# Kernel tuning notes

Measured on AMD Instinct MI355X. Metric: run time of the kernel, lower is better.

Reference implementation:

```python
import jax, jax.numpy as jnp
import numpy as np

EPS = 1e-5


def setup_inputs() -> dict:
    key = jax.random.key(0)
    S, B, I, H, D = 256, 512, 64, 128, 32
    ks = jax.random.split(key, 12)

    def w(k, shape, fan):
        return jax.random.normal(k, shape, jnp.float32) * (fan ** -0.5)

    lengths = jax.random.randint(ks[0], (B,), 1, S + 1)
    lengths = lengths.at[0].set(S)  # ensure max length == S
    return {
        'x': jax.random.normal(ks[1], (S, B, I), jnp.float32),
        'x_d': jax.random.normal(ks[2], (S, B, D), jnp.float32),
        'lengths': lengths,
        'bn_g': jnp.ones((I,), jnp.float32), 'bn_b': jnp.zeros((I,), jnp.float32),
        'bnd_g': jnp.ones((D,), jnp.float32), 'bnd_b': jnp.zeros((D,), jnp.float32),
        'Wih': w(ks[3], (3 * H, I), I), 'Whh': w(ks[4], (3 * H, H), H),
        'bih': jnp.zeros((3 * H,), jnp.float32), 'bhh': jnp.zeros((3 * H,), jnp.float32),
        'attn_W': w(ks[5], (H, H), H), 'attn_b': jnp.zeros((H,), jnp.float32),
        'W1': w(ks[6], (H, H + D), H + D), 'b1': jnp.zeros((H,), jnp.float32),
        'W2': w(ks[7], (H, H), H), 'b2': jnp.zeros((H,), jnp.float32),
        'W3': w(ks[8], (H, H), H), 'b3': jnp.zeros((H,), jnp.float32),
    }


def reference(x, x_d, lengths, bn_g, bn_b, bnd_g, bnd_b, Wih, Whh, bih, bhh,
              attn_W, attn_b, W1, b1, W2, b2, W3, b3):
    S, B, I = x.shape
    H = Whh.shape[1]
    mask = jnp.arange(S)[:, None] < lengths[None, :]          # [S,B] valid-token mask
    mf = mask[..., None].astype(x.dtype)                       # [S,B,1]
    cnt = mf.sum()

    def bn(v, g, b):  # training-mode BatchNorm1d over the packed (valid) tokens
        mu = (v * mf).sum((0, 1)) / cnt
        var = (((v - mu) * mf) ** 2).sum((0, 1)) / cnt
        return (v - mu) * jax.lax.rsqrt(var + EPS) * g + b

    xn = bn(x, bn_g, bn_b)
    xdn = bn(x_d, bnd_g, bnd_b)

    # --- GRU (PyTorch gate order r,z,n) over padded sequence with mask ---
    h0 = jnp.zeros((B, H), x.dtype)

    def step(h, inp):
        xt, mt = inp                                           # xt [B,I], mt [B,1]
        gi = xt @ Wih.T + bih
        gh = h @ Whh.T + bhh
        ir, iz, inn = jnp.split(gi, 3, axis=-1)
        hr, hz, hn = jnp.split(gh, 3, axis=-1)
        r = jax.nn.sigmoid(ir + hr)
        z = jax.nn.sigmoid(iz + hz)
        n = jnp.tanh(inn + r * hn)
        hnew = (1 - z) * n + z * h
        hnext = jnp.where(mt, hnew, h)                         # carry last valid state
        return hnext, jnp.where(mt, hnew, 0.0)                 # padded outputs are 0

    h_last, ys = jax.lax.scan(step, h0, (xn, mf))              # ys [S,B,H]

    # --- Dynamic_Attention: per step i only position j=i survives the causal
    # mask in column k=i, so the dim-0 softmax is over one element -> weight 1.
    # Keep fc in the graph (zero grad, same as torch) via a size-1 softmax. ---
    s = (ys @ attn_W.T + attn_b).sum(-1)                       # [S,B]
    attn = jax.nn.softmax(s[..., None, None], axis=-2)[..., 0, :]  # ones [S,B,1]
    y = attn * ys

    # --- per-token MLP (dropout = identity at eval), vectorized over all tokens ---
    z0 = jnp.concatenate([y, xdn], axis=-1)                    # [S,B,H+D]
    d = jax.nn.relu(z0 @ W1.T + b1)
    d = jax.nn.relu(d @ W2.T + b2)
    d = jax.nn.relu(d @ W3.T + b3)
    out = d * mf                                               # zero padded positions
    return out, h_last[None]                                   # hidden: [1,B,H]
```

## Files before the change

kernel.cpp:

```cpp
#include <hip/hip_runtime.h>
#include <hip/hip_bf16.h>

#define SS 256
#define BB 512
#define II 64
#define HH 128
#define DD 32

typedef __attribute__((ext_vector_type(8))) short short8;
typedef __attribute__((ext_vector_type(4))) float f32x4;

__device__ __forceinline__ short f2bf(float f) {
    unsigned u = __builtin_bit_cast(unsigned, f);
    u += 0x7FFFu + ((u >> 16) & 1u);
    return (short)(u >> 16);
}
__device__ __forceinline__ int pack2bf(float a, float b) {
    return (int)((((unsigned)(unsigned short)f2bf(b)) << 16) |
                  ((unsigned)(unsigned short)f2bf(a)));
}
__device__ __forceinline__ short8 load8bf(const float* p) {
    short8 r;
#pragma unroll
    for (int j = 0; j < 8; ++j) r[j] = f2bf(p[j]);
    return r;
}

__device__ __forceinline__ void sync_lds() {
    __builtin_amdgcn_s_waitcnt(0xc07f);
    __builtin_amdgcn_s_barrier();
}

__global__ __launch_bounds__(256) void stats_kernel(
    const float* __restrict__ x, const float* __restrict__ xd,
    const int* __restrict__ lengths, double* __restrict__ acc,
    unsigned* __restrict__ counter,
    const float* __restrict__ bn_g, const float* __restrict__ bn_b,
    const float* __restrict__ bnd_g, const float* __restrict__ bnd_b,
    float* __restrict__ der)
{
    __shared__ int s_len[BB];
    __shared__ f32x4 red_s[256];
    __shared__ f32x4 red_q[256];
    __shared__ unsigned s_last;

    const int tid = threadIdx.x;
    const int blk = blockIdx.x;
    for (int i = tid; i < BB; i += 256) s_len[i] = lengths[i];
    __syncthreads();

    f32x4 s = {0.f, 0.f, 0.f, 0.f};
    f32x4 q = {0.f, 0.f, 0.f, 0.f};

    if (blk < 256) {
        const int c4   = tid & 15;
        const int rowg = tid >> 4;
        const float* base = x + (size_t)blk * BB * II + c4 * 4;
#pragma unroll 8
        for (int it = 0; it < 32; ++it) {
            const int b = it * 16 + rowg;
            const f32x4 xv = *(const f32x4*)&base[(size_t)b * II];
            const f32x4 xm = (blk < s_len[b]) ? xv : (f32x4){0.f, 0.f, 0.f, 0.f};
            s += xm;
            q += xm * xm;
        }
        red_s[tid] = s; red_q[tid] = q;
        __syncthreads();
#pragma unroll
        for (int g = 8; g >= 1; g >>= 1) {
            if (rowg < g) {
                red_s[tid] += red_s[tid + 16 * g];
                red_q[tid] += red_q[tid + 16 * g];
            }
            __syncthreads();
        }
        if (rowg == 0) {
            const f32x4 fs = red_s[tid], fq = red_q[tid];
#pragma unroll
            for (int j = 0; j < 4; ++j) {
                atomicAdd(&acc[c4 * 4 + j],      (double)fs[j]);
                atomicAdd(&acc[64 + c4 * 4 + j], (double)fq[j]);
            }
        }
    } else {
        const int bx   = blk - 256;
        const int c4   = tid & 7;
        const int rowg = tid >> 3;
        const int r0   = bx * 1024;
        const float* base = xd + (size_t)r0 * DD + c4 * 4;
#pragma unroll 8
        for (int it = 0; it < 32; ++it) {
            const int rr  = it * 32 + rowg;
            const int row = r0 + rr;
            const int b   = row & (BB - 1);
            const int si  = row >> 9;
            const f32x4 xv = *(const f32x4*)&base[(size_t)rr * DD];
            const f32x4 xm = (si < s_len[b]) ? xv : (f32x4){0.f, 0.f, 0.f, 0.f};
            s += xm;
            q += xm * xm;
        }
        red_s[tid] = s; red_q[tid] = q;
        __syncthreads();
#pragma unroll
        for (int g = 16; g >= 1; g >>= 1) {
            if (rowg < g) {
                red_s[tid] += red_s[tid + 8 * g];
                red_q[tid] += red_q[tid + 8 * g];
            }
            __syncthreads();
        }
        if (rowg == 0) {
            const f32x4 fs = red_s[tid], fq = red_q[tid];
#pragma unroll
            for (int j = 0; j < 4; ++j) {
                atomicAdd(&acc[128 + c4 * 4 + j], (double)fs[j]);
                atomicAdd(&acc[160 + c4 * 4 + j], (double)fq[j]);
            }
        }
    }

    __threadfence();
    __syncthreads();
    if (tid == 0) {
        unsigned old = atomicAdd(counter, 1u);
        s_last = (old == 383u) ? 1u : 0u;
    }
    __syncthreads();
    if (!s_last) return;

    __shared__ int redc[256];
    int cs = 0;
    for (int i = tid; i < BB; i += 256) cs += s_len[i];
    redc[tid] = cs;
    __syncthreads();
    for (int off = 128; off; off >>= 1) {
        if (tid < off) redc[tid] += redc[tid + off];
        __syncthreads();
    }
    const double inv = 1.0 / (double)redc[0];
    if (tid < 64) {
        const double su = __hip_atomic_load(&acc[tid],      __ATOMIC_RELAXED, __HIP_MEMORY_SCOPE_AGENT);
        const double sq = __hip_atomic_load(&acc[64 + tid], __ATOMIC_RELAXED, __HIP_MEMORY_SCOPE_AGENT);
        const double mu  = su * inv;
        const double var = sq * inv - mu * mu;
        const float  rs  = rsqrtf((float)(var + 1e-5));
        const float  a   = rs * bn_g[tid];
        der[tid]      = a;
        der[64 + tid] = bn_b[tid] - (float)mu * a;
    } else if (tid < 96) {
        const int i = tid - 64;
        const double su = __hip_atomic_load(&acc[128 + i], __ATOMIC_RELAXED, __HIP_MEMORY_SCOPE_AGENT);
        const double sq = __hip_atomic_load(&acc[160 + i], __ATOMIC_RELAXED, __HIP_MEMORY_SCOPE_AGENT);
        const double mu  = su * inv;
        const double var = sq * inv - mu * mu;
        const float  rs  = rsqrtf((float)(var + 1e-5));
        const float  a   = rs * bnd_g[i];
        der[128 + i] = a;
        der[160 + i] = bnd_b[i] - (float)mu * a;
    }
}

__global__ __launch_bounds__(512, 2) void gru_kernel(
    const float* __restrict__ x, const int* __restrict__ lengths,
    const float* __restrict__ Wih, const float* __restrict__ Whh,
    const float* __restrict__ bih, const float* __restrict__ bhh,
    const float* __restrict__ der,
    float* __restrict__ ys, float* __restrict__ hlast)
{
    __shared__ __align__(16) short hbf[2][16 * 136];
    __shared__ __align__(16) short xbf[2][16 * 72];

    const int tid  = threadIdx.x;
    const int w    = tid >> 6;
    const int l    = tid & 63;
    const int col  = l & 15;
    const int quad = l >> 4;
    const int b0   = blockIdx.x * 16;
    const int ur   = 16 * w + col;
    const int g0   = 16 * w + quad * 4;

    short8 WR[6], WZ[6], WNh[4], WNx[2];
#pragma unroll
    for (int ks = 0; ks < 4; ++ks) {
        const int ko = ks * 32 + quad * 8;
        WR[ks]  = load8bf(&Whh[(size_t)ur * HH + ko]);
        WZ[ks]  = load8bf(&Whh[(size_t)(HH + ur) * HH + ko]);
        WNh[ks] = load8bf(&Whh[(size_t)(2 * HH + ur) * HH + ko]);
    }
#pragma unroll
    for (int ks = 0; ks < 2; ++ks) {
        const int ko = ks * 32 + quad * 8;
        WR[4 + ks] = load8bf(&Wih[(size_t)ur * II + ko]);
        WZ[4 + ks] = load8bf(&Wih[(size_t)(HH + ur) * II + ko]);
        WNx[ks]    = load8bf(&Wih[(size_t)(2 * HH + ur) * II + ko]);
    }
    float br_[4], bz_[4], bnh_[4], bnx_[4];
#pragma unroll
    for (int r = 0; r < 4; ++r) {
        const int g = g0 + r;
        br_[r]  = bih[g] + bhh[g];
        bz_[r]  = bih[HH + g] + bhh[HH + g];
        bnh_[r] = bhh[2 * HH + g];
        bnx_[r] = bih[2 * HH + g];
    }
    const int len = lengths[b0 + col];

    const int srow = tid >> 5, scol = (tid & 31) * 2;
    const float ax0 = der[scol],      ax1 = der[scol + 1];
    const float cx0 = der[64 + scol], cx1 = der[64 + scol + 1];

    for (int i = tid; i < 16 * 136 / 2; i += 512) ((int*)hbf[0])[i] = 0;
    float hreg[4] = {0.f, 0.f, 0.f, 0.f};
    {
        const float2 xv = *(const float2*)&x[(size_t)(b0 + srow) * II + scol];
        *(int*)&xbf[0][srow * 72 + scol] =
            pack2bf(fmaf(xv.x, ax0, cx0), fmaf(xv.y, ax1, cx1));
    }
    sync_lds();

    int p = 0;
    for (int t = 0; t < SS; ++t) {
        float2 xv;
        if (t + 1 < SS)
            xv = *(const float2*)&x[(size_t)((t + 1) * BB + b0 + srow) * II + scol];

        short8 Hf[4];
#pragma unroll
        for (int ks = 0; ks < 4; ++ks)
            Hf[ks] = *(const short8*)&hbf[p][col * 136 + ks * 32 + quad * 8];
        const short8 XN0 = *(const short8*)&xbf[p][col * 72 + quad * 8];
        const short8 XN1 = *(const short8*)&xbf[p][col * 72 + 32 + quad * 8];

        f32x4 ar  = {br_[0],  br_[1],  br_[2],  br_[3]};
        f32x4 az  = {bz_[0],  bz_[1],  bz_[2],  bz_[3]};
        f32x4 anh = {bnh_[0], bnh_[1], bnh_[2], bnh_[3]};
        f32x4 anx = {bnx_[0], bnx_[1], bnx_[2], bnx_[3]};
#pragma unroll
        for (int ks = 0; ks < 4; ++ks) {
            ar  = __builtin_amdgcn_mfma_f32_16x16x32_bf16(WR[ks],  Hf[ks], ar,  0, 0, 0);
            az  = __builtin_amdgcn_mfma_f32_16x16x32_bf16(WZ[ks],  Hf[ks], az,  0, 0, 0);
            anh = __builtin_amdgcn_mfma_f32_16x16x32_bf16(WNh[ks], Hf[ks], anh, 0, 0, 0);
        }
        ar  = __builtin_amdgcn_mfma_f32_16x16x32_bf16(WR[4],  XN0, ar,  0, 0, 0);
        ar  = __builtin_amdgcn_mfma_f32_16x16x32_bf16(WR[5],  XN1, ar,  0, 0, 0);
        az  = __builtin_amdgcn_mfma_f32_16x16x32_bf16(WZ[4],  XN0, az,  0, 0, 0);
        az  = __builtin_amdgcn_mfma_f32_16x16x32_bf16(WZ[5],  XN1, az,  0, 0, 0);
        anx = __builtin_amdgcn_mfma_f32_16x16x32_bf16(WNx[0], XN0, anx, 0, 0, 0);
        anx = __builtin_amdgcn_mfma_f32_16x16x32_bf16(WNx[1], XN1, anx, 0, 0, 0);

        const bool valid = (t < len);
#pragma unroll
        for (int r = 0; r < 4; ++r) {
            const float rg = __builtin_amdgcn_rcpf(1.f + __expf(-ar[r]));
            const float zg = __builtin_amdgcn_rcpf(1.f + __expf(-az[r]));
            const float nv = anx[r] + rg * anh[r];
            const float ng = 1.f - 2.f * __builtin_amdgcn_rcpf(1.f + __expf(2.f * nv));
            const float hnew = (1.f - zg) * ng + zg * hreg[r];
            hreg[r] = valid ? hnew : hreg[r];
        }
        {
            float4 o;
            o.x = hreg[0]; o.y = hreg[1]; o.z = hreg[2]; o.w = hreg[3];
            *(float4*)&ys[((size_t)t * BB + b0 + col) * HH + g0] = o;
            int2 pk;
            pk.x = pack2bf(hreg[0], hreg[1]);
            pk.y = pack2bf(hreg[2], hreg[3]);
            *(int2*)&hbf[p ^ 1][col * 136 + g0] = pk;
        }
        if (t + 1 < SS)
            *(int*)&xbf[p ^ 1][srow * 72 + scol] =
                pack2bf(fmaf(xv.x, ax0, cx0), fmaf(xv.y, ax1, cx1));

        sync_lds();
        p ^= 1;
    }

    {
        float4 hl;
        hl.x = hreg[0]; hl.y = hreg[1]; hl.z = hreg[2]; hl.w = hreg[3];
        *(float4*)&hlast[(size_t)(b0 + col) * HH + g0] = hl;
    }
}

__global__ __launch_bounds__(512, 2) void mlp_kernel(
    const float* __restrict__ xd, const int* __restrict__ lengths,
    const float* __restrict__ W1, const float* __restrict__ b1v,
    const float* __restrict__ W2, const float* __restrict__ b2v,
    const float* __restrict__ W3, const float* __restrict__ b3v,
    const float* __restrict__ der, float* io)
{
    __shared__ __align__(16) short z0[2][16 * 168];
    __shared__ __align__(16) short d1b[2][16 * 136];
    __shared__ __align__(16) short d2b[2][16 * 136];

    const int tid  = threadIdx.x;
    const int w    = tid >> 6;
    const int l    = tid & 63;
    const int col  = l & 15;
    const int quad = l >> 4;
    const int ur   = 16 * w + col;
    const int g0   = 16 * w + quad * 4;

    short8 F1[5], F2[4], F3[4];
#pragma unroll
    for (int ks = 0; ks < 5; ++ks)
        F1[ks] = load8bf(&W1[(size_t)ur * 160 + ks * 32 + quad * 8]);
#pragma unroll
    for (int ks = 0; ks < 4; ++ks) {
        const int ko = ks * 32 + quad * 8;
        F2[ks] = load8bf(&W2[(size_t)ur * HH + ko]);
        F3[ks] = load8bf(&W3[(size_t)ur * HH + ko]);
    }
    float bb1_[4], bb2_[4], bb3_[4];
#pragma unroll
    for (int r = 0; r < 4; ++r) {
        bb1_[r] = b1v[g0 + r]; bb2_[r] = b2v[g0 + r]; bb3_[r] = b3v[g0 + r];
    }

    const int yrow = tid >> 5, yc = (tid & 31) * 4;
    const int drow = tid >> 4, dcol = (tid & 15) * 2;
    float ad0 = 0.f, ad1 = 0.f, cd0 = 0.f, cd1 = 0.f;
    if (tid < 256) {
        ad0 = der[128 + dcol]; ad1 = der[128 + dcol + 1];
        cd0 = der[160 + dcol]; cd1 = der[160 + dcol + 1];
    }

    const int tile0 = blockIdx.x * 16;

    {
        const size_t tok0 = (size_t)tile0 * 16;
        const float4 yv = *(const float4*)&io[(tok0 + yrow) * HH + yc];
        int2 pk;
        pk.x = pack2bf(yv.x, yv.y);
        pk.y = pack2bf(yv.z, yv.w);
        *(int2*)&z0[0][yrow * 168 + yc] = pk;
        if (tid < 256) {
            const float2 dv = *(const float2*)&xd[(tok0 + drow) * DD + dcol];
            *(int*)&z0[0][drow * 168 + HH + dcol] =
                pack2bf(fmaf(dv.x, ad0, cd0), fmaf(dv.y, ad1, cd1));
        }
    }
    sync_lds();

    int p = 0;
    for (int it = 0; it <= 17; ++it) {
        float4 yv; float2 dv;
        const int nt = it + 1;
        if (nt <= 15) {
            const size_t tok0n = (size_t)(tile0 + nt) * 16;
            yv = *(const float4*)&io[(tok0n + yrow) * HH + yc];
            if (tid < 256) dv = *(const float2*)&xd[(tok0n + drow) * DD + dcol];
        }

        f32x4 a1 = {bb1_[0], bb1_[1], bb1_[2], bb1_[3]};
#pragma unroll
        for (int ks = 0; ks < 5; ++ks)
            a1 = __builtin_amdgcn_mfma_f32_16x16x32_bf16(
                F1[ks], *(const short8*)&z0[p][col * 168 + ks * 32 + quad * 8], a1, 0, 0, 0);
        {
            int2 pk;
            pk.x = pack2bf(fmaxf(a1[0], 0.f), fmaxf(a1[1], 0.f));
            pk.y = pack2bf(fmaxf(a1[2], 0.f), fmaxf(a1[3], 0.f));
            *(int2*)&d1b[p ^ 1][col * 136 + g0] = pk;
        }

        f32x4 a2 = {bb2_[0], bb2_[1], bb2_[2], bb2_[3]};
#pragma unroll
        for (int ks = 0; ks < 4; ++ks)
            a2 = __builtin_amdgcn_mfma_f32_16x16x32_bf16(
                F2[ks], *(const short8*)&d1b[p][col * 136 + ks * 32 + quad * 8], a2, 0, 0, 0);
        {
            int2 pk;
            pk.x = pack2bf(fmaxf(a2[0], 0.f), fmaxf(a2[1], 0.f));
            pk.y = pack2bf(fmaxf(a2[2], 0.f), fmaxf(a2[3], 0.f));
            *(int2*)&d2b[p ^ 1][col * 136 + g0] = pk;
        }

        f32x4 a3 = {bb3_[0], bb3_[1], bb3_[2], bb3_[3]};
#pragma unroll
        for (int ks = 0; ks < 4; ++ks)
            a3 = __builtin_amdgcn_mfma_f32_16x16x32_bf16(
                F3[ks], *(const short8*)&d2b[p][col * 136 + ks * 32 + quad * 8], a3, 0, 0, 0);
        if (it >= 2) {
            const int tok0 = (tile0 + it - 2) * 16;
            const int tI = tok0 >> 9;
            const int bI = tok0 & (BB - 1);
            const bool v = tI < lengths[bI + col];
            float4 o;
            o.x = v ? fmaxf(a3[0], 0.f) : 0.f;
            o.y = v ? fmaxf(a3[1], 0.f) : 0.f;
            o.z = v ? fmaxf(a3[2], 0.f) : 0.f;
            o.w = v ? fmaxf(a3[3], 0.f) : 0.f;
            *(float4*)&io[((size_t)tok0 + col) * HH + g0] = o;
        }

        if (nt <= 15) {
            int2 pk;
            pk.x = pack2bf(yv.x, yv.y);
            pk.y = pack2bf(yv.z, yv.w);
            *(int2*)&z0[p ^ 1][yrow * 168 + yc] = pk;
            if (tid < 256)
                *(int*)&z0[p ^ 1][drow * 168 + HH + dcol] =
                    pack2bf(fmaf(dv.x, ad0, cd0), fmaf(dv.y, ad1, cd1));
        }
        sync_lds();
        p ^= 1;
    }
}

extern "C" void kernel_launch(void* const* d_in, const int* in_sizes, int n_in,
                              void* d_out, int out_size, void* d_ws, size_t ws_size,
                              hipStream_t stream)
{
    (void)in_sizes; (void)n_in; (void)out_size; (void)ws_size;
    const float* x     = (const float*)d_in[0];
    const float* xd    = (const float*)d_in[1];
    const int*   lens  = (const int*)d_in[2];
    const float* bn_g  = (const float*)d_in[3];
    const float* bn_b  = (const float*)d_in[4];
    const float* bnd_g = (const float*)d_in[5];
    const float* bnd_b = (const float*)d_in[6];
    const float* Wih   = (const float*)d_in[7];
    const float* Whh   = (const float*)d_in[8];
    const float* bih   = (const float*)d_in[9];
    const float* bhh   = (const float*)d_in[10];
    const float* W1    = (const float*)d_in[13];
    const float* b1    = (const float*)d_in[14];
    const float* W2    = (const float*)d_in[15];
    const float* b2    = (const float*)d_in[16];
    const float* W3    = (const float*)d_in[17];
    const float* b3    = (const float*)d_in[18];

    float* out   = (float*)d_out;
    float* hlast = out + (size_t)SS * BB * HH;

    double*   acc     = (double*)d_ws;
    unsigned* counter = (unsigned*)((char*)d_ws + 1536);
    float*    der     = (float*)((char*)d_ws + 2048);

    (void)hipMemsetAsync(d_ws, 0, 2048, stream);

    stats_kernel<<<384, 256, 0, stream>>>(x, xd, lens, acc, counter,
                                          bn_g, bn_b, bnd_g, bnd_b, der);

    gru_kernel<<<BB / 16, 512, 0, stream>>>(x, lens, Wih, Whh, bih, bhh, der,
                                            out, hlast);

    mlp_kernel<<<512, 512, 0, stream>>>(xd, lens, W1, b1, W2, b2, W3, b3,
                                        der, out);
}
```

Before: 428.8 us.

## Fuse GRU and MLP into one persistent kernel with progress-flag overlap

Merges the GRU and MLP kernels into a single launch. 32 blocks run the recurrence and publish per-block progress counters every 16 timesteps. The remaining 448 blocks spin on those counters and run the MLP on finished time tiles while the recurrence continues, so most of the MLP overlaps the serial GRU. The stats kernel also replaces double atomics with per-block partial sums that the last block reduces. The overlap relies on every GRU block being co-resident with the MLP blocks and uses spin-waits, which risks deadlock or contention with the GRU blocks.

```diff
diff --git a/kernel.cpp b/kernel.cpp
--- a/kernel.cpp
+++ b/kernel.cpp
@@ -33,7 +33,8 @@
 
 __global__ __launch_bounds__(256) void stats_kernel(
     const float* __restrict__ x, const float* __restrict__ xd,
-    const int* __restrict__ lengths, double* __restrict__ acc,
+    const int* __restrict__ lengths,
+    float* __restrict__ px, float* __restrict__ pd,
     unsigned* __restrict__ counter,
     const float* __restrict__ bn_g, const float* __restrict__ bn_b,
     const float* __restrict__ bnd_g, const float* __restrict__ bnd_b,
@@ -76,10 +77,11 @@
         }
         if (rowg == 0) {
             const f32x4 fs = red_s[tid], fq = red_q[tid];
+            float* row = px + (size_t)blk * 128;
 #pragma unroll
             for (int j = 0; j < 4; ++j) {
-                atomicAdd(&acc[c4 * 4 + j],      (double)fs[j]);
-                atomicAdd(&acc[64 + c4 * 4 + j], (double)fq[j]);
+                __hip_atomic_store(&row[c4 * 4 + j],      fs[j], __ATOMIC_RELAXED, __HIP_MEMORY_SCOPE_AGENT);
+                __hip_atomic_store(&row[64 + c4 * 4 + j], fq[j], __ATOMIC_RELAXED, __HIP_MEMORY_SCOPE_AGENT);
             }
         }
     } else {
@@ -111,10 +113,11 @@
         }
         if (rowg == 0) {
             const f32x4 fs = red_s[tid], fq = red_q[tid];
+            float* row = pd + (size_t)bx * 64;
 #pragma unroll
             for (int j = 0; j < 4; ++j) {
-                atomicAdd(&acc[128 + c4 * 4 + j], (double)fs[j]);
-                atomicAdd(&acc[160 + c4 * 4 + j], (double)fq[j]);
+                __hip_atomic_store(&row[c4 * 4 + j],      fs[j], __ATOMIC_RELAXED, __HIP_MEMORY_SCOPE_AGENT);
+                __hip_atomic_store(&row[32 + c4 * 4 + j], fq[j], __ATOMIC_RELAXED, __HIP_MEMORY_SCOPE_AGENT);
             }
         }
     }
@@ -127,7 +130,24 @@
     }
     __syncthreads();
     if (!s_last) return;
-
+    __threadfence();
+
+    __shared__ double s_sum[192];
+    if (tid < 128) {
+        const float* col = px + tid;
+        double a = 0.0;
+#pragma unroll 8
+        for (int r = 0; r < 256; ++r)
+            a += (double)__hip_atomic_load(&col[(size_t)r * 128], __ATOMIC_RELAXED, __HIP_MEMORY_SCOPE_AGENT);
+        s_sum[tid] = a;
+    } else if (tid < 192) {
+        const float* col = pd + (tid - 128);
+        double a = 0.0;
+#pragma unroll 8
+        for (int r = 0; r < 128; ++r)
+            a += (double)__hip_atomic_load(&col[(size_t)r * 64], __ATOMIC_RELAXED, __HIP_MEMORY_SCOPE_AGENT);
+        s_sum[tid] = a;
+    }
     __shared__ int redc[256];
     int cs = 0;
     for (int i = tid; i < BB; i += 256) cs += s_len[i];
@@ -139,20 +159,16 @@
     }
     const double inv = 1.0 / (double)redc[0];
     if (tid < 64) {
-        const double su = __hip_atomic_load(&acc[tid],      __ATOMIC_RELAXED, __HIP_MEMORY_SCOPE_AGENT);
-        const double sq = __hip_atomic_load(&acc[64 + tid], __ATOMIC_RELAXED, __HIP_MEMORY_SCOPE_AGENT);
-        const double mu  = su * inv;
-        const double var = sq * inv - mu * mu;
+        const double mu  = s_sum[tid] * inv;
+        const double var = s_sum[64 + tid] * inv - mu * mu;
         const float  rs  = rsqrtf((float)(var + 1e-5));
         const float  a   = rs * bn_g[tid];
         der[tid]      = a;
         der[64 + tid] = bn_b[tid] - (float)mu * a;
     } else if (tid < 96) {
         const int i = tid - 64;
-        const double su = __hip_atomic_load(&acc[128 + i], __ATOMIC_RELAXED, __HIP_MEMORY_SCOPE_AGENT);
-        const double sq = __hip_atomic_load(&acc[160 + i], __ATOMIC_RELAXED, __HIP_MEMORY_SCOPE_AGENT);
-        const double mu  = su * inv;
-        const double var = sq * inv - mu * mu;
+        const double mu  = s_sum[128 + i] * inv;
+        const double var = s_sum[160 + i] * inv - mu * mu;
         const float  rs  = rsqrtf((float)(var + 1e-5));
         const float  a   = rs * bnd_g[i];
         der[128 + i] = a;
@@ -160,139 +176,19 @@
     }
 }
 
-__global__ __launch_bounds__(512, 2) void gru_kernel(
-    const float* __restrict__ x, const int* __restrict__ lengths,
+__global__ __launch_bounds__(512, 4) void fused_kernel(
+    const float* __restrict__ x, const float* __restrict__ xd,
+    const int* __restrict__ lengths,
     const float* __restrict__ Wih, const float* __restrict__ Whh,
     const float* __restrict__ bih, const float* __restrict__ bhh,
-    const float* __restrict__ der,
-    float* __restrict__ ys, float* __restrict__ hlast)
-{
-    __shared__ __align__(16) short hbf[2][16 * 136];
-    __shared__ __align__(16) short xbf[2][16 * 72];
-
-    const int tid  = threadIdx.x;
-    const int w    = tid >> 6;
-    const int l    = tid & 63;
-    const int col  = l & 15;
-    const int quad = l >> 4;
-    const int b0   = blockIdx.x * 16;
-    const int ur   = 16 * w + col;
-    const int g0   = 16 * w + quad * 4;
-
-    short8 WR[6], WZ[6], WNh[4], WNx[2];
-#pragma unroll
-    for (int ks = 0; ks < 4; ++ks) {
-        const int ko = ks * 32 + quad * 8;
-        WR[ks]  = load8bf(&Whh[(size_t)ur * HH + ko]);
-        WZ[ks]  = load8bf(&Whh[(size_t)(HH + ur) * HH + ko]);
-        WNh[ks] = load8bf(&Whh[(size_t)(2 * HH + ur) * HH + ko]);
-    }
-#pragma unroll
-    for (int ks = 0; ks < 2; ++ks) {
-        const int ko = ks * 32 + quad * 8;
-        WR[4 + ks] = load8bf(&Wih[(size_t)ur * II + ko]);
-        WZ[4 + ks] = load8bf(&Wih[(size_t)(HH + ur) * II + ko]);
-        WNx[ks]    = load8bf(&Wih[(size_t)(2 * HH + ur) * II + ko]);
-    }
-    float br_[4], bz_[4], bnh_[4], bnx_[4];
-#pragma unroll
-    for (int r = 0; r < 4; ++r) {
-        const int g = g0 + r;
-        br_[r]  = bih[g] + bhh[g];
-        bz_[r]  = bih[HH + g] + bhh[HH + g];
-        bnh_[r] = bhh[2 * HH + g];
-        bnx_[r] = bih[2 * HH + g];
-    }
-    const int len = lengths[b0 + col];
-
-    const int srow = tid >> 5, scol = (tid & 31) * 2;
-    const float ax0 = der[scol],      ax1 = der[scol + 1];
-    const float cx0 = der[64 + scol], cx1 = der[64 + scol + 1];
-
-    for (int i = tid; i < 16 * 136 / 2; i += 512) ((int*)hbf[0])[i] = 0;
-    float hreg[4] = {0.f, 0.f, 0.f, 0.f};
-    {
-        const float2 xv = *(const float2*)&x[(size_t)(b0 + srow) * II + scol];
-        *(int*)&xbf[0][srow * 72 + scol] =
-            pack2bf(fmaf(xv.x, ax0, cx0), fmaf(xv.y, ax1, cx1));
-    }
-    sync_lds();
-
-    int p = 0;
-    for (int t = 0; t < SS; ++t) {
-        float2 xv;
-        if (t + 1 < SS)
-            xv = *(const float2*)&x[(size_t)((t + 1) * BB + b0 + srow) * II + scol];
-
-        short8 Hf[4];
-#pragma unroll
-        for (int ks = 0; ks < 4; ++ks)
-            Hf[ks] = *(const short8*)&hbf[p][col * 136 + ks * 32 + quad * 8];
-        const short8 XN0 = *(const short8*)&xbf[p][col * 72 + quad * 8];
-        const short8 XN1 = *(const short8*)&xbf[p][col * 72 + 32 + quad * 8];
-
-        f32x4 ar  = {br_[0],  br_[1],  br_[2],  br_[3]};
-        f32x4 az  = {bz_[0],  bz_[1],  bz_[2],  bz_[3]};
-        f32x4 anh = {bnh_[0], bnh_[1], bnh_[2], bnh_[3]};
-        f32x4 anx = {bnx_[0], bnx_[1], bnx_[2], bnx_[3]};
-#pragma unroll
-        for (int ks = 0; ks < 4; ++ks) {
-            ar  = __builtin_amdgcn_mfma_f32_16x16x32_bf16(WR[ks],  Hf[ks], ar,  0, 0, 0);
-            az  = __builtin_amdgcn_mfma_f32_16x16x32_bf16(WZ[ks],  Hf[ks], az,  0, 0, 0);
-            anh = __builtin_amdgcn_mfma_f32_16x16x32_bf16(WNh[ks], Hf[ks], anh, 0, 0, 0);
-        }
-        ar  = __builtin_amdgcn_mfma_f32_16x16x32_bf16(WR[4],  XN0, ar,  0, 0, 0);
-        ar  = __builtin_amdgcn_mfma_f32_16x16x32_bf16(WR[5],  XN1, ar,  0, 0, 0);
-        az  = __builtin_amdgcn_mfma_f32_16x16x32_bf16(WZ[4],  XN0, az,  0, 0, 0);
-        az  = __builtin_amdgcn_mfma_f32_16x16x32_bf16(WZ[5],  XN1, az,  0, 0, 0);
-        anx = __builtin_amdgcn_mfma_f32_16x16x32_bf16(WNx[0], XN0, anx, 0, 0, 0);
-        anx = __builtin_amdgcn_mfma_f32_16x16x32_bf16(WNx[1], XN1, anx, 0, 0, 0);
-
-        const bool valid = (t < len);
-#pragma unroll
-        for (int r = 0; r < 4; ++r) {
-            const float rg = __builtin_amdgcn_rcpf(1.f + __expf(-ar[r]));
-            const float zg = __builtin_amdgcn_rcpf(1.f + __expf(-az[r]));
-            const float nv = anx[r] + rg * anh[r];
-            const float ng = 1.f - 2.f * __builtin_amdgcn_rcpf(1.f + __expf(2.f * nv));
-            const float hnew = (1.f - zg) * ng + zg * hreg[r];
-            hreg[r] = valid ? hnew : hreg[r];
-        }
-        {
-            float4 o;
-            o.x = hreg[0]; o.y = hreg[1]; o.z = hreg[2]; o.w = hreg[3];
-            *(float4*)&ys[((size_t)t * BB + b0 + col) * HH + g0] = o;
-            int2 pk;
-            pk.x = pack2bf(hreg[0], hreg[1]);
-            pk.y = pack2bf(hreg[2], hreg[3]);
-            *(int2*)&hbf[p ^ 1][col * 136 + g0] = pk;
-        }
-        if (t + 1 < SS)
-            *(int*)&xbf[p ^ 1][srow * 72 + scol] =
-                pack2bf(fmaf(xv.x, ax0, cx0), fmaf(xv.y, ax1, cx1));
-
-        sync_lds();
-        p ^= 1;
-    }
-
-    {
-        float4 hl;
-        hl.x = hreg[0]; hl.y = hreg[1]; hl.z = hreg[2]; hl.w = hreg[3];
-        *(float4*)&hlast[(size_t)(b0 + col) * HH + g0] = hl;
-    }
-}
-
-__global__ __launch_bounds__(512, 2) void mlp_kernel(
-    const float* __restrict__ xd, const int* __restrict__ lengths,
     const float* __restrict__ W1, const float* __restrict__ b1v,
     const float* __restrict__ W2, const float* __restrict__ b2v,
     const float* __restrict__ W3, const float* __restrict__ b3v,
-    const float* __restrict__ der, float* io)
+    const float* __restrict__ der,
+    float* __restrict__ out, float* __restrict__ hlast,
+    int* __restrict__ prog)
 {
-    __shared__ __align__(16) short z0[2][16 * 168];
-    __shared__ __align__(16) short d1b[2][16 * 136];
-    __shared__ __align__(16) short d2b[2][16 * 136];
-
+    __shared__ __align__(16) char smem[28160];
     const int tid  = threadIdx.x;
     const int w    = tid >> 6;
     const int l    = tid & 63;
@@ -301,110 +197,248 @@
     const int ur   = 16 * w + col;
     const int g0   = 16 * w + quad * 4;
 
-    short8 F1[5], F2[4], F3[4];
-#pragma unroll
-    for (int ks = 0; ks < 5; ++ks)
-        F1[ks] = load8bf(&W1[(size_t)ur * 160 + ks * 32 + quad * 8]);
-#pragma unroll
-    for (int ks = 0; ks < 4; ++ks) {
-        const int ko = ks * 32 + quad * 8;
-        F2[ks] = load8bf(&W2[(size_t)ur * HH + ko]);
-        F3[ks] = load8bf(&W3[(size_t)ur * HH + ko]);
-    }
-    float bb1_[4], bb2_[4], bb3_[4];
-#pragma unroll
-    for (int r = 0; r < 4; ++r) {
-        bb1_[r] = b1v[g0 + r]; bb2_[r] = b2v[g0 + r]; bb3_[r] = b3v[g0 + r];
-    }
-
-    const int yrow = tid >> 5, yc = (tid & 31) * 4;
-    const int drow = tid >> 4, dcol = (tid & 15) * 2;
-    float ad0 = 0.f, ad1 = 0.f, cd0 = 0.f, cd1 = 0.f;
-    if (tid < 256) {
-        ad0 = der[128 + dcol]; ad1 = der[128 + dcol + 1];
-        cd0 = der[160 + dcol]; cd1 = der[160 + dcol + 1];
-    }
-
-    const int tile0 = blockIdx.x * 16;
-
-    {
-        const size_t tok0 = (size_t)tile0 * 16;
-        const float4 yv = *(const float4*)&io[(tok0 + yrow) * HH + yc];
-        int2 pk;
-        pk.x = pack2bf(yv.x, yv.y);
-        pk.y = pack2bf(yv.z, yv.w);
-        *(int2*)&z0[0][yrow * 168 + yc] = pk;
+    if (blockIdx.x < 32) {
+        __builtin_amdgcn_s_setprio(2);
+        short (*hbf)[16 * 136] = reinterpret_cast<short (*)[16 * 136]>(smem);
+        short (*xbf)[16 * 72]  = reinterpret_cast<short (*)[16 * 72]>(smem + 8704);
+
+        const int bid = blockIdx.x;
+        const int b0  = bid * 16;
+
+        short8 WR[6], WZ[6], WNh[4], WNx[2];
+#pragma unroll
+        for (int ks = 0; ks < 4; ++ks) {
+            const int ko = ks * 32 + quad * 8;
+            WR[ks]  = load8bf(&Whh[(size_t)ur * HH + ko]);
+            WZ[ks]  = load8bf(&Whh[(size_t)(HH + ur) * HH + ko]);
+            WNh[ks] = load8bf(&Whh[(size_t)(2 * HH + ur) * HH + ko]);
+        }
+#pragma unroll
+        for (int ks = 0; ks < 2; ++ks) {
+            const int ko = ks * 32 + quad * 8;
+            WR[4 + ks] = load8bf(&Wih[(size_t)ur * II + ko]);
+            WZ[4 + ks] = load8bf(&Wih[(size_t)(HH + ur) * II + ko]);
+            WNx[ks]    = load8bf(&Wih[(size_t)(2 * HH + ur) * II + ko]);
+        }
+        float br_[4], bz_[4], bnh_[4], bnx_[4];
+#pragma unroll
+        for (int r = 0; r < 4; ++r) {
+            const int g = g0 + r;
+            br_[r]  = bih[g] + bhh[g];
+            bz_[r]  = bih[HH + g] + bhh[HH + g];
+            bnh_[r] = bhh[2 * HH + g];
+            bnx_[r] = bih[2 * HH + g];
+        }
+        const int len = lengths[b0 + col];
+
+        const int srow = tid >> 5, scol = (tid & 31) * 2;
+        const float ax0 = der[scol],      ax1 = der[scol + 1];
+        const float cx0 = der[64 + scol], cx1 = der[64 + scol + 1];
+
+        for (int i = tid; i < 16 * 136 / 2; i += 512) ((int*)hbf[0])[i] = 0;
+        float hreg[4] = {0.f, 0.f, 0.f, 0.f};
+        {
+            const float2 xv = *(const float2*)&x[(size_t)(b0 + srow) * II + scol];
+            *(int*)&xbf[0][srow * 72 + scol] =
+                pack2bf(fmaf(xv.x, ax0, cx0), fmaf(xv.y, ax1, cx1));
+        }
+        sync_lds();
+
+        int p = 0;
+        for (int t = 0; t < SS; ++t) {
+            float2 xv;
+            if (t + 1 < SS)
+                xv = *(const float2*)&x[(size_t)((t + 1) * BB + b0 + srow) * II + scol];
+
+            short8 Hf[4];
+#pragma unroll
+            for (int ks = 0; ks < 4; ++ks)
+                Hf[ks] = *(const short8*)&hbf[p][col * 136 + ks * 32 + quad * 8];
+            const short8 XN0 = *(const short8*)&xbf[p][col * 72 + quad * 8];
+            const short8 XN1 = *(const short8*)&xbf[p][col * 72 + 32 + quad * 8];
+
+            f32x4 ar  = {br_[0],  br_[1],  br_[2],  br_[3]};
+            f32x4 az  = {bz_[0],  bz_[1],  bz_[2],  bz_[3]};
+            f32x4 anh = {bnh_[0], bnh_[1], bnh_[2], bnh_[3]};
+            f32x4 anx = {bnx_[0], bnx_[1], bnx_[2], bnx_[3]};
+#pragma unroll
+            for (int ks = 0; ks < 4; ++ks) {
+                ar  = __builtin_amdgcn_mfma_f32_16x16x32_bf16(WR[ks],  Hf[ks], ar,  0, 0, 0);
+                az  = __builtin_amdgcn_mfma_f32_16x16x32_bf16(WZ[ks],  Hf[ks], az,  0, 0, 0);
+                anh = __builtin_amdgcn_mfma_f32_16x16x32_bf16(WNh[ks], Hf[ks], anh, 0, 0, 0);
+            }
+            ar  = __builtin_amdgcn_mfma_f32_16x16x32_bf16(WR[4],  XN0, ar,  0, 0, 0);
+            ar  = __builtin_amdgcn_mfma_f32_16x16x32_bf16(WR[5],  XN1, ar,  0, 0, 0);
+            az  = __builtin_amdgcn_mfma_f32_16x16x32_bf16(WZ[4],  XN0, az,  0, 0, 0);
+            az  = __builtin_amdgcn_mfma_f32_16x16x32_bf16(WZ[5],  XN1, az,  0, 0, 0);
+            anx = __builtin_amdgcn_mfma_f32_16x16x32_bf16(WNx[0], XN0, anx, 0, 0, 0);
+            anx = __builtin_amdgcn_mfma_f32_16x16x32_bf16(WNx[1], XN1, anx, 0, 0, 0);
+
+            const bool valid = (t < len);
+#pragma unroll
+            for (int r = 0; r < 4; ++r) {
+                const float rg = __builtin_amdgcn_rcpf(1.f + __expf(-ar[r]));
+                const float zg = __builtin_amdgcn_rcpf(1.f + __expf(-az[r]));
+                const float nv = anx[r] + rg * anh[r];
+                const float ng = 1.f - 2.f * __builtin_amdgcn_rcpf(1.f + __expf(2.f * nv));
+                const float hnew = (1.f - zg) * ng + zg * hreg[r];
+                hreg[r] = valid ? hnew : hreg[r];
+            }
+            {
+                float4 o;
+                o.x = hreg[0]; o.y = hreg[1]; o.z = hreg[2]; o.w = hreg[3];
+                *(float4*)&out[((size_t)t * BB + b0 + col) * HH + g0] = o;
+                int2 pk;
+                pk.x = pack2bf(hreg[0], hreg[1]);
+                pk.y = pack2bf(hreg[2], hreg[3]);
+                *(int2*)&hbf[p ^ 1][col * 136 + g0] = pk;
+            }
+            if (t + 1 < SS)
+                *(int*)&xbf[p ^ 1][srow * 72 + scol] =
+                    pack2bf(fmaf(xv.x, ax0, cx0), fmaf(xv.y, ax1, cx1));
+
+            if ((t & 15) == 15) {
+                asm volatile("s_waitcnt vmcnt(0)" ::: "memory");
+                sync_lds();
+                if (tid == 0) {
+                    __threadfence();
+                    __hip_atomic_store(&prog[bid], t + 1,
+                                       __ATOMIC_RELEASE, __HIP_MEMORY_SCOPE_AGENT);
+                }
+            } else {
+                sync_lds();
+            }
+            p ^= 1;
+        }
+
+        {
+            float4 hl;
+            hl.x = hreg[0]; hl.y = hreg[1]; hl.z = hreg[2]; hl.w = hreg[3];
+            *(float4*)&hlast[(size_t)(b0 + col) * HH + g0] = hl;
+        }
+    } else {
+        short (*z0)[16 * 168]  = reinterpret_cast<short (*)[16 * 168]>(smem);
+        short (*d1b)[16 * 136] = reinterpret_cast<short (*)[16 * 136]>(smem + 10752);
+        short (*d2b)[16 * 136] = reinterpret_cast<short (*)[16 * 136]>(smem + 19456);
+
+        const int j = blockIdx.x - 32;
+
+        short8 F1[5], F2[4], F3[4];
+#pragma unroll
+        for (int ks = 0; ks < 5; ++ks)
+            F1[ks] = load8bf(&W1[(size_t)ur * 160 + ks * 32 + quad * 8]);
+#pragma unroll
+        for (int ks = 0; ks < 4; ++ks) {
+            const int ko = ks * 32 + quad * 8;
+            F2[ks] = load8bf(&W2[(size_t)ur * HH + ko]);
+            F3[ks] = load8bf(&W3[(size_t)ur * HH + ko]);
+        }
+        float bb1_[4], bb2_[4], bb3_[4];
+#pragma unroll
+        for (int r = 0; r < 4; ++r) {
+            bb1_[r] = b1v[g0 + r]; bb2_[r] = b2v[g0 + r]; bb3_[r] = b3v[g0 + r];
+        }
+        const int yrow = tid >> 5, yc = (tid & 31) * 4;
+        const int drow = tid >> 4, dcol = (tid & 15) * 2;
+        float ad0 = 0.f, ad1 = 0.f, cd0 = 0.f, cd1 = 0.f;
         if (tid < 256) {
-            const float2 dv = *(const float2*)&xd[(tok0 + drow) * DD + dcol];
-            *(int*)&z0[0][drow * 168 + HH + dcol] =
-                pack2bf(fmaf(dv.x, ad0, cd0), fmaf(dv.y, ad1, cd1));
-        }
-    }
-    sync_lds();
-
-    int p = 0;
-    for (int it = 0; it <= 17; ++it) {
-        float4 yv; float2 dv;
-        const int nt = it + 1;
-        if (nt <= 15) {
-            const size_t tok0n = (size_t)(tile0 + nt) * 16;
-            yv = *(const float4*)&io[(tok0n + yrow) * HH + yc];
-            if (tid < 256) dv = *(const float2*)&xd[(tok0n + drow) * DD + dcol];
-        }
-
-        f32x4 a1 = {bb1_[0], bb1_[1], bb1_[2], bb1_[3]};
-#pragma unroll
-        for (int ks = 0; ks < 5; ++ks)
-            a1 = __builtin_amdgcn_mfma_f32_16x16x32_bf16(
-                F1[ks], *(const short8*)&z0[p][col * 168 + ks * 32 + quad * 8], a1, 0, 0, 0);
-        {
-            int2 pk;
-            pk.x = pack2bf(fmaxf(a1[0], 0.f), fmaxf(a1[1], 0.f));
-            pk.y = pack2bf(fmaxf(a1[2], 0.f), fmaxf(a1[3], 0.f));
-            *(int2*)&d1b[p ^ 1][col * 136 + g0] = pk;
-        }
-
-        f32x4 a2 = {bb2_[0], bb2_[1], bb2_[2], bb2_[3]};
-#pragma unroll
-        for (int ks = 0; ks < 4; ++ks)
-            a2 = __builtin_amdgcn_mfma_f32_16x16x32_bf16(
-                F2[ks], *(const short8*)&d1b[p][col * 136 + ks * 32 + quad * 8], a2, 0, 0, 0);
-        {
-            int2 pk;
-            pk.x = pack2bf(fmaxf(a2[0], 0.f), fmaxf(a2[1], 0.f));
-            pk.y = pack2bf(fmaxf(a2[2], 0.f), fmaxf(a2[3], 0.f));
-            *(int2*)&d2b[p ^ 1][col * 136 + g0] = pk;
-        }
-
-        f32x4 a3 = {bb3_[0], bb3_[1], bb3_[2], bb3_[3]};
-#pragma unroll
-        for (int ks = 0; ks < 4; ++ks)
-            a3 = __builtin_amdgcn_mfma_f32_16x16x32_bf16(
-                F3[ks], *(const short8*)&d2b[p][col * 136 + ks * 32 + quad * 8], a3, 0, 0, 0);
-        if (it >= 2) {
-            const int tok0 = (tile0 + it - 2) * 16;
-            const int tI = tok0 >> 9;
-            const int bI = tok0 & (BB - 1);
-            const bool v = tI < lengths[bI + col];
-            float4 o;
-            o.x = v ? fmaxf(a3[0], 0.f) : 0.f;
-            o.y = v ? fmaxf(a3[1], 0.f) : 0.f;
-            o.z = v ? fmaxf(a3[2], 0.f) : 0.f;
-            o.w = v ? fmaxf(a3[3], 0.f) : 0.f;
-            *(float4*)&io[((size_t)tok0 + col) * HH + g0] = o;
-        }
-
-        if (nt <= 15) {
-            int2 pk;
-            pk.x = pack2bf(yv.x, yv.y);
-            pk.y = pack2bf(yv.z, yv.w);
-            *(int2*)&z0[p ^ 1][yrow * 168 + yc] = pk;
-            if (tid < 256)
-                *(int*)&z0[p ^ 1][drow * 168 + HH + dcol] =
-                    pack2bf(fmaf(dv.x, ad0, cd0), fmaf(dv.y, ad1, cd1));
-        }
-        sync_lds();
-        p ^= 1;
+            ad0 = der[128 + dcol]; ad1 = der[128 + dcol + 1];
+            cd0 = der[160 + dcol]; cd1 = der[160 + dcol + 1];
+        }
+
+        for (int c = j; c < 512; c += 448) {
+            const int tneed = c >> 1;
+            const int gbase = (c & 1) * 16;
+            if (tid < 16) {
+                while (__hip_atomic_load(&prog[gbase + tid], __ATOMIC_ACQUIRE,
+                                         __HIP_MEMORY_SCOPE_AGENT) <= tneed)
+                    __builtin_amdgcn_s_sleep(32);
+            }
+            __syncthreads();
+
+            const int tile0 = c * 16;
+            {
+                const size_t tok0 = (size_t)tile0 * 16;
+                const float4 yv = *(const float4*)&out[(tok0 + yrow) * HH + yc];
+                int2 pk;
+                pk.x = pack2bf(yv.x, yv.y);
+                pk.y = pack2bf(yv.z, yv.w);
+                *(int2*)&z0[0][yrow * 168 + yc] = pk;
+                if (tid < 256) {
+                    const float2 dv = *(const float2*)&xd[(tok0 + drow) * DD + dcol];
+                    *(int*)&z0[0][drow * 168 + HH + dcol] =
+                        pack2bf(fmaf(dv.x, ad0, cd0), fmaf(dv.y, ad1, cd1));
+                }
+            }
+            sync_lds();
+
+            int p = 0;
+            for (int it = 0; it <= 17; ++it) {
+                float4 yv; float2 dv;
+                const int nt = it + 1;
+                if (nt <= 15) {
+                    const size_t tok0n = (size_t)(tile0 + nt) * 16;
+                    yv = *(const float4*)&out[(tok0n + yrow) * HH + yc];
+                    if (tid < 256) dv = *(const float2*)&xd[(tok0n + drow) * DD + dcol];
+                }
+
+                f32x4 a1 = {bb1_[0], bb1_[1], bb1_[2], bb1_[3]};
+#pragma unroll
+                for (int ks = 0; ks < 5; ++ks)
+                    a1 = __builtin_amdgcn_mfma_f32_16x16x32_bf16(
+                        F1[ks], *(const short8*)&z0[p][col * 168 + ks * 32 + quad * 8], a1, 0, 0, 0);
+                {
+                    int2 pk;
+                    pk.x = pack2bf(fmaxf(a1[0], 0.f), fmaxf(a1[1], 0.f));
+                    pk.y = pack2bf(fmaxf(a1[2], 0.f), fmaxf(a1[3], 0.f));
+                    *(int2*)&d1b[p ^ 1][col * 136 + g0] = pk;
+                }
+
+                f32x4 a2 = {bb2_[0], bb2_[1], bb2_[2], bb2_[3]};
+#pragma unroll
+                for (int ks = 0; ks < 4; ++ks)
+                    a2 = __builtin_amdgcn_mfma_f32_16x16x32_bf16(
+                        F2[ks], *(const short8*)&d1b[p][col * 136 + ks * 32 + quad * 8], a2, 0, 0, 0);
+                {
+                    int2 pk;
+                    pk.x = pack2bf(fmaxf(a2[0], 0.f), fmaxf(a2[1], 0.f));
+                    pk.y = pack2bf(fmaxf(a2[2], 0.f), fmaxf(a2[3], 0.f));
+                    *(int2*)&d2b[p ^ 1][col * 136 + g0] = pk;
+                }
+
+                f32x4 a3 = {bb3_[0], bb3_[1], bb3_[2], bb3_[3]};
+#pragma unroll
+                for (int ks = 0; ks < 4; ++ks)
+                    a3 = __builtin_amdgcn_mfma_f32_16x16x32_bf16(
+                        F3[ks], *(const short8*)&d2b[p][col * 136 + ks * 32 + quad * 8], a3, 0, 0, 0);
+                if (it >= 2) {
+                    const int tok0 = (tile0 + it - 2) * 16;
+                    const int tI = tok0 >> 9;
+                    const int bI = tok0 & (BB - 1);
+                    const bool v = tI < lengths[bI + col];
+                    float4 o;
+                    o.x = v ? fmaxf(a3[0], 0.f) : 0.f;
+                    o.y = v ? fmaxf(a3[1], 0.f) : 0.f;
+                    o.z = v ? fmaxf(a3[2], 0.f) : 0.f;
+                    o.w = v ? fmaxf(a3[3], 0.f) : 0.f;
+                    *(float4*)&out[((size_t)tok0 + col) * HH + g0] = o;
+                }
+
+                if (nt <= 15) {
+                    int2 pk;
+                    pk.x = pack2bf(yv.x, yv.y);
+                    pk.y = pack2bf(yv.z, yv.w);
+                    *(int2*)&z0[p ^ 1][yrow * 168 + yc] = pk;
+                    if (tid < 256)
+                        *(int*)&z0[p ^ 1][drow * 168 + HH + dcol] =
+                            pack2bf(fmaf(dv.x, ad0, cd0), fmaf(dv.y, ad1, cd1));
+                }
+                sync_lds();
+                p ^= 1;
+            }
+            asm volatile("s_waitcnt vmcnt(0)" ::: "memory");
+            __syncthreads();
+        }
     }
 }
 
@@ -434,18 +468,18 @@
     float* out   = (float*)d_out;
     float* hlast = out + (size_t)SS * BB * HH;
 
-    double*   acc     = (double*)d_ws;
-    unsigned* counter = (unsigned*)((char*)d_ws + 1536);
-    float*    der     = (float*)((char*)d_ws + 2048);
+    unsigned* counter  = (unsigned*)((char*)d_ws + 1536);
+    int*      prog     = (int*)((char*)d_ws + 1792);
+    float*    der      = (float*)((char*)d_ws + 2048);
+    float*    px       = (float*)((char*)d_ws + 4096);
+    float*    pd       = px + 256 * 128;
 
     (void)hipMemsetAsync(d_ws, 0, 2048, stream);
 
-    stats_kernel<<<384, 256, 0, stream>>>(x, xd, lens, acc, counter,
+    stats_kernel<<<384, 256, 0, stream>>>(x, xd, lens, px, pd, counter,
                                           bn_g, bn_b, bnd_g, bnd_b, der);
 
-    gru_kernel<<<BB / 16, 512, 0, stream>>>(x, lens, Wih, Whh, bih, bhh, der,
-                                            out, hlast);
-
-    mlp_kernel<<<512, 512, 0, stream>>>(xd, lens, W1, b1, W2, b2, W3, b3,
-                                        der, out);
-}
+    fused_kernel<<<480, 512, 0, stream>>>(x, xd, lens, Wih, Whh, bih, bhh,
+                                          W1, b1, W2, b2, W3, b3,
+                                          der, out, hlast, prog);
+}
```

New measurement: 1.571 ms. 3.66x slower.

## Swizzle LDS tiles with XOR and replace double atomics with per-block partials

Applied to the files above, without the earlier changes.

The stats kernel stops issuing double-precision atomicAdds into shared accumulators. Each block now stores its float partial sums to its own row of a workspace buffer, and the last block to finish reduces those rows in double. Separately, the padded LDS row strides (136 and 72) in the GRU and MLP kernels become unpadded strides (128 and 64) with an XOR swizzle on the 8-element column groups. This keeps LDS accesses free of bank conflicts while using less shared memory. The cost is a serial reduction of up to 256 rows done by one block at the end of the stats kernel.

```diff
diff --git a/kernel.cpp b/kernel.cpp
--- a/kernel.cpp
+++ b/kernel.cpp
@@ -31,9 +31,12 @@
     __builtin_amdgcn_s_barrier();
 }
 
+#define SWZ(colv, off) ((off) ^ (((colv) & 7) << 3))
+
 __global__ __launch_bounds__(256) void stats_kernel(
     const float* __restrict__ x, const float* __restrict__ xd,
-    const int* __restrict__ lengths, double* __restrict__ acc,
+    const int* __restrict__ lengths,
+    float* __restrict__ px, float* __restrict__ pd,
     unsigned* __restrict__ counter,
     const float* __restrict__ bn_g, const float* __restrict__ bn_b,
     const float* __restrict__ bnd_g, const float* __restrict__ bnd_b,
@@ -76,10 +79,11 @@
         }
         if (rowg == 0) {
             const f32x4 fs = red_s[tid], fq = red_q[tid];
+            float* row = px + (size_t)blk * 128;
 #pragma unroll
             for (int j = 0; j < 4; ++j) {
-                atomicAdd(&acc[c4 * 4 + j],      (double)fs[j]);
-                atomicAdd(&acc[64 + c4 * 4 + j], (double)fq[j]);
+                __hip_atomic_store(&row[c4 * 4 + j],      fs[j], __ATOMIC_RELAXED, __HIP_MEMORY_SCOPE_AGENT);
+                __hip_atomic_store(&row[64 + c4 * 4 + j], fq[j], __ATOMIC_RELAXED, __HIP_MEMORY_SCOPE_AGENT);
             }
         }
     } else {
@@ -111,10 +115,11 @@
         }
         if (rowg == 0) {
             const f32x4 fs = red_s[tid], fq = red_q[tid];
+            float* row = pd + (size_t)bx * 64;
 #pragma unroll
             for (int j = 0; j < 4; ++j) {
-                atomicAdd(&acc[128 + c4 * 4 + j], (double)fs[j]);
-                atomicAdd(&acc[160 + c4 * 4 + j], (double)fq[j]);
+                __hip_atomic_store(&row[c4 * 4 + j],      fs[j], __ATOMIC_RELAXED, __HIP_MEMORY_SCOPE_AGENT);
+                __hip_atomic_store(&row[32 + c4 * 4 + j], fq[j], __ATOMIC_RELAXED, __HIP_MEMORY_SCOPE_AGENT);
             }
         }
     }
@@ -127,7 +132,24 @@
     }
     __syncthreads();
     if (!s_last) return;
-
+    __threadfence();
+
+    __shared__ double s_sum[192];
+    if (tid < 128) {
+        const float* col = px + tid;
+        double a = 0.0;
+#pragma unroll 8
+        for (int r = 0; r < 256; ++r)
+            a += (double)__hip_atomic_load(&col[(size_t)r * 128], __ATOMIC_RELAXED, __HIP_MEMORY_SCOPE_AGENT);
+        s_sum[tid] = a;
+    } else if (tid < 192) {
+        const float* col = pd + (tid - 128);
+        double a = 0.0;
+#pragma unroll 8
+        for (int r = 0; r < 128; ++r)
+            a += (double)__hip_atomic_load(&col[(size_t)r * 64], __ATOMIC_RELAXED, __HIP_MEMORY_SCOPE_AGENT);
+        s_sum[tid] = a;
+    }
     __shared__ int redc[256];
     int cs = 0;
     for (int i = tid; i < BB; i += 256) cs += s_len[i];
@@ -139,20 +161,16 @@
     }
     const double inv = 1.0 / (double)redc[0];
     if (tid < 64) {
-        const double su = __hip_atomic_load(&acc[tid],      __ATOMIC_RELAXED, __HIP_MEMORY_SCOPE_AGENT);
-        const double sq = __hip_atomic_load(&acc[64 + tid], __ATOMIC_RELAXED, __HIP_MEMORY_SCOPE_AGENT);
-        const double mu  = su * inv;
-        const double var = sq * inv - mu * mu;
+        const double mu  = s_sum[tid] * inv;
+        const double var = s_sum[64 + tid] * inv - mu * mu;
         const float  rs  = rsqrtf((float)(var + 1e-5));
         const float  a   = rs * bn_g[tid];
         der[tid]      = a;
         der[64 + tid] = bn_b[tid] - (float)mu * a;
     } else if (tid < 96) {
         const int i = tid - 64;
-        const double su = __hip_atomic_load(&acc[128 + i], __ATOMIC_RELAXED, __HIP_MEMORY_SCOPE_AGENT);
-        const double sq = __hip_atomic_load(&acc[160 + i], __ATOMIC_RELAXED, __HIP_MEMORY_SCOPE_AGENT);
-        const double mu  = su * inv;
-        const double var = sq * inv - mu * mu;
+        const double mu  = s_sum[128 + i] * inv;
+        const double var = s_sum[160 + i] * inv - mu * mu;
         const float  rs  = rsqrtf((float)(var + 1e-5));
         const float  a   = rs * bnd_g[i];
         der[128 + i] = a;
@@ -167,8 +185,8 @@
     const float* __restrict__ der,
     float* __restrict__ ys, float* __restrict__ hlast)
 {
-    __shared__ __align__(16) short hbf[2][16 * 136];
-    __shared__ __align__(16) short xbf[2][16 * 72];
+    __shared__ __align__(16) short hbf[2][16 * 128];
+    __shared__ __align__(16) short xbf[2][16 * 64];
 
     const int tid  = threadIdx.x;
     const int w    = tid >> 6;
@@ -209,11 +227,11 @@
     const float ax0 = der[scol],      ax1 = der[scol + 1];
     const float cx0 = der[64 + scol], cx1 = der[64 + scol + 1];
 
-    for (int i = tid; i < 16 * 136 / 2; i += 512) ((int*)hbf[0])[i] = 0;
+    for (int i = tid; i < 16 * 128 / 2; i += 512) ((int*)hbf[0])[i] = 0;
     float hreg[4] = {0.f, 0.f, 0.f, 0.f};
     {
         const float2 xv = *(const float2*)&x[(size_t)(b0 + srow) * II + scol];
-        *(int*)&xbf[0][srow * 72 + scol] =
+        *(int*)&xbf[0][SWZ(srow, srow * 64 + scol)] =
             pack2bf(fmaf(xv.x, ax0, cx0), fmaf(xv.y, ax1, cx1));
     }
     sync_lds();
@@ -227,9 +245,9 @@
         short8 Hf[4];
 #pragma unroll
         for (int ks = 0; ks < 4; ++ks)
-            Hf[ks] = *(const short8*)&hbf[p][col * 136 + ks * 32 + quad * 8];
-        const short8 XN0 = *(const short8*)&xbf[p][col * 72 + quad * 8];
-        const short8 XN1 = *(const short8*)&xbf[p][col * 72 + 32 + quad * 8];
+            Hf[ks] = *(const short8*)&hbf[p][SWZ(col, col * 128 + ks * 32 + quad * 8)];
+        const short8 XN0 = *(const short8*)&xbf[p][SWZ(col, col * 64 + quad * 8)];
+        const short8 XN1 = *(const short8*)&xbf[p][SWZ(col, col * 64 + 32 + quad * 8)];
 
         f32x4 ar  = {br_[0],  br_[1],  br_[2],  br_[3]};
         f32x4 az  = {bz_[0],  bz_[1],  bz_[2],  bz_[3]};
@@ -265,10 +283,10 @@
             int2 pk;
             pk.x = pack2bf(hreg[0], hreg[1]);
             pk.y = pack2bf(hreg[2], hreg[3]);
-            *(int2*)&hbf[p ^ 1][col * 136 + g0] = pk;
+            *(int2*)&hbf[p ^ 1][SWZ(col, col * 128 + g0)] = pk;
         }
         if (t + 1 < SS)
-            *(int*)&xbf[p ^ 1][srow * 72 + scol] =
+            *(int*)&xbf[p ^ 1][SWZ(srow, srow * 64 + scol)] =
                 pack2bf(fmaf(xv.x, ax0, cx0), fmaf(xv.y, ax1, cx1));
 
         sync_lds();
@@ -290,8 +308,8 @@
     const float* __restrict__ der, float* io)
 {
     __shared__ __align__(16) short z0[2][16 * 168];
-    __shared__ __align__(16) short d1b[2][16 * 136];
-    __shared__ __align__(16) short d2b[2][16 * 136];
+    __shared__ __align__(16) short d1b[2][16 * 128];
+    __shared__ __align__(16) short d2b[2][16 * 128];
 
     const int tid  = threadIdx.x;
     const int w    = tid >> 6;
@@ -361,26 +379,26 @@
             int2 pk;
             pk.x = pack2bf(fmaxf(a1[0], 0.f), fmaxf(a1[1], 0.f));
             pk.y = pack2bf(fmaxf(a1[2], 0.f), fmaxf(a1[3], 0.f));
-            *(int2*)&d1b[p ^ 1][col * 136 + g0] = pk;
+            *(int2*)&d1b[p ^ 1][SWZ(col, col * 128 + g0)] = pk;
         }
 
         f32x4 a2 = {bb2_[0], bb2_[1], bb2_[2], bb2_[3]};
 #pragma unroll
         for (int ks = 0; ks < 4; ++ks)
             a2 = __builtin_amdgcn_mfma_f32_16x16x32_bf16(
-                F2[ks], *(const short8*)&d1b[p][col * 136 + ks * 32 + quad * 8], a2, 0, 0, 0);
+                F2[ks], *(const short8*)&d1b[p][SWZ(col, col * 128 + ks * 32 + quad * 8)], a2, 0, 0, 0);
         {
             int2 pk;
             pk.x = pack2bf(fmaxf(a2[0], 0.f), fmaxf(a2[1], 0.f));
             pk.y = pack2bf(fmaxf(a2[2], 0.f), fmaxf(a2[3], 0.f));
-            *(int2*)&d2b[p ^ 1][col * 136 + g0] = pk;
+            *(int2*)&d2b[p ^ 1][SWZ(col, col * 128 + g0)] = pk;
         }
 
         f32x4 a3 = {bb3_[0], bb3_[1], bb3_[2], bb3_[3]};
 #pragma unroll
         for (int ks = 0; ks < 4; ++ks)
             a3 = __builtin_amdgcn_mfma_f32_16x16x32_bf16(
-                F3[ks], *(const short8*)&d2b[p][col * 136 + ks * 32 + quad * 8], a3, 0, 0, 0);
+                F3[ks], *(const short8*)&d2b[p][SWZ(col, col * 128 + ks * 32 + quad * 8)], a3, 0, 0, 0);
         if (it >= 2) {
             const int tok0 = (tile0 + it - 2) * 16;
             const int tI = tok0 >> 9;
@@ -412,7 +430,7 @@
                               void* d_out, int out_size, void* d_ws, size_t ws_size,
                               hipStream_t stream)
 {
-    (void)in_sizes; (void)n_in; (void)out_size; (void)ws_size;
+    (void)in_sizes; (void)n_in; (void)out_size;
     const float* x     = (const float*)d_in[0];
     const float* xd    = (const float*)d_in[1];
     const int*   lens  = (const int*)d_in[2];
@@ -434,13 +452,14 @@
     float* out   = (float*)d_out;
     float* hlast = out + (size_t)SS * BB * HH;
 
-    double*   acc     = (double*)d_ws;
-    unsigned* counter = (unsigned*)((char*)d_ws + 1536);
-    float*    der     = (float*)((char*)d_ws + 2048);
+    unsigned* counter  = (unsigned*)((char*)d_ws + 1536);
+    float*    der      = (float*)((char*)d_ws + 2048);
+    float*    px       = (float*)((char*)d_ws + 4096);
+    float*    pd       = px + 256 * 128;
 
     (void)hipMemsetAsync(d_ws, 0, 2048, stream);
 
-    stats_kernel<<<384, 256, 0, stream>>>(x, xd, lens, acc, counter,
+    stats_kernel<<<384, 256, 0, stream>>>(x, xd, lens, px, pd, counter,
                                           bn_g, bn_b, bnd_g, bnd_b, der);
 
     gru_kernel<<<BB / 16, 512, 0, stream>>>(x, lens, Wih, Whh, bih, bhh, der,
```

New measurement: 446.1 us. 4.0% more time.
